# Performance work log

Measured on AMD Instinct MI355X. Metric: run time of the kernel, lower is better.

The kernel has to match this reference:

```python
import jax, jax.numpy as jnp
import numpy as np

B, M, D1, D2 = 1, 2048, 128, 16
NQ, NK, H, DH = 32, 128, 8, 16


def _build_index(M, nq, nk):
    """Replicates AttentionIndex._create_attention_idx (numpy)."""
    half = (nq - 1.0) * 0.5
    centers = np.round(np.arange(half, M + half, nq, dtype=np.float32)).astype(np.int64)
    C = len(centers)
    query_idx = np.arange(M, dtype=np.int64)
    pad = np.full(C * nq - M, -1, dtype=np.int64)
    query_idx = np.concatenate([query_idx, pad]).reshape(C, nq)
    query_mask = (query_idx != -1).astype(np.int64)
    query_idx = query_idx * query_mask
    key_idx = np.full((C, nk), -1, dtype=np.int64)
    for i, c in enumerate(centers):
        s = max(int(c) - nk // 2, 0)
        e = min(int(c) + nk // 2, M)
        key_idx[i, : e - s] = np.arange(s, e, dtype=np.int64)
    key_mask = (key_idx != -1).astype(np.int64)
    key_idx = key_idx * key_mask
    alpha_mask = query_mask[:, :, None] * key_mask[:, None, :]
    # valid slots hold flat pair index q*M + k, zero elsewhere (matches np.put_along_axis path)
    pair_idx = (query_idx[:, :, None] * M + key_idx[:, None, :]) * alpha_mask
    return query_idx, query_mask, key_idx, key_mask, alpha_mask, pair_idx


def setup_inputs() -> dict:
    key = jax.random.key(0)
    ks = jax.random.split(key, 8)
    qi, qm, ki, km, am, pi = _build_index(M, NQ, NK)
    s = 0.02
    return {
        "ql": jax.random.normal(ks[0], (B, M, D1), jnp.float32),
        "cl": jax.random.normal(ks[1], (B, M, D1), jnp.float32),
        "plm": jax.random.normal(ks[2], (B, M, M, D2), jnp.float32),
        "Wq": jax.random.normal(ks[3], (D1, H * DH), jnp.float32) * s,
        "Wk": jax.random.normal(ks[4], (D1, H * DH), jnp.float32) * s,
        "Wv": jax.random.normal(ks[5], (D1, H * DH), jnp.float32) * s,
        "Wb": jax.random.normal(ks[6], (D2, H), jnp.float32) * s,
        "Wo": jax.random.normal(ks[7], (H * DH, D1), jnp.float32) * s,
        "query_idx": jnp.asarray(qi),
        "query_mask": jnp.asarray(qm),
        "key_idx": jnp.asarray(ki),
        "key_mask": jnp.asarray(km),
        "alpha_mask": jnp.asarray(am),
        "pair_idx": jnp.asarray(pi),
    }


def _ln(x):
    mu = jnp.mean(x, axis=-1, keepdims=True)
    var = jnp.var(x, axis=-1, keepdims=True)
    return (x - mu) * jax.lax.rsqrt(var + 1e-5)


def reference(ql, cl, plm, Wq, Wk, Wv, Wb, Wo,
              query_idx, query_mask, key_idx, key_mask, alpha_mask, pair_idx):
    Bn, Mn, _ = ql.shape
    C, nq = query_idx.shape
    nk = key_idx.shape[1]
    # beta bias: 0 at valid (q,k) pairs, -1e10 at masked slots (per AtomTransformer.forward)
    beta = jnp.where(alpha_mask == 1, 0.0, -1e10).astype(ql.dtype)  # (C,nq,nk)

    q = (_ln(ql) @ Wq).reshape(Bn, Mn, H, DH)
    kv = _ln(cl)
    k = (kv @ Wk).reshape(Bn, Mn, H, DH)
    v = (kv @ Wv).reshape(Bn, Mn, H, DH)

    qw = q[:, query_idx]  # (B,C,nq,H,DH)  gather query windows
    kw = k[:, key_idx]    # (B,C,nk,H,DH)  gather key windows
    vw = v[:, key_idx]    # (B,C,nk,H,DH)

    # per-pair bias: gather plm rows via precomputed flat pair_idx
    pw = plm.reshape(Bn, Mn * Mn, D2)[:, pair_idx.reshape(-1)]
    pw = pw.reshape(Bn, C, nq, nk, D2)
    bias = jnp.moveaxis(pw @ Wb, -1, 1)  # (B,H,C,nq,nk)

    scores = jnp.einsum("bcqhd,bckhd->bhcqk", qw, kw) / np.float32(np.sqrt(DH))
    scores = scores + bias + beta[None, None]
    attn = jax.nn.softmax(scores, axis=-1)
    ow = jnp.einsum("bhcqk,bckhd->bcqhd", attn, vw)

    # scatter window outputs back to atoms (query windows tile [0,M))
    ow = ow.reshape(Bn, C * nq, H * DH) * query_mask.reshape(1, C * nq, 1).astype(ow.dtype)
    o = jnp.zeros((Bn, Mn, H * DH), ow.dtype).at[:, query_idx.reshape(-1)].add(ow)
    return ql + o @ Wo
```

## Files before the change

### kernel.cpp

```cpp
#include <hip/hip_runtime.h>
#include <math.h>

#define MDIM 2048
#define D1C  128
#define D2C  16
#define NQC  32
#define NKC  128
#define HC   8
#define DHC  16
#define CC   64

__global__ __launch_bounds__(256) void ln_proj_kernel(
    const float* __restrict__ ql, const float* __restrict__ cl,
    const float* __restrict__ Wq, const float* __restrict__ Wk,
    const float* __restrict__ Wv,
    float* __restrict__ qbuf, float* __restrict__ kbuf, float* __restrict__ vbuf)
{
    __shared__ float ldsQ[8 * 128];
    __shared__ float ldsC[8 * 128];
    const int tid = threadIdx.x;
    const int rg = tid >> 5;
    const int t  = tid & 31;
    const int m  = blockIdx.x * 8 + rg;

    const float4 xq = reinterpret_cast<const float4*>(ql)[m * 32 + t];
    const float4 xc = reinterpret_cast<const float4*>(cl)[m * 32 + t];
    float sQ  = xq.x + xq.y + xq.z + xq.w;
    float sqQ = xq.x*xq.x + xq.y*xq.y + xq.z*xq.z + xq.w*xq.w;
    float sC  = xc.x + xc.y + xc.z + xc.w;
    float sqC = xc.x*xc.x + xc.y*xc.y + xc.z*xc.z + xc.w*xc.w;
    #pragma unroll
    for (int msk = 16; msk; msk >>= 1) {
        sQ  += __shfl_xor(sQ,  msk);
        sqQ += __shfl_xor(sqQ, msk);
        sC  += __shfl_xor(sC,  msk);
        sqC += __shfl_xor(sqC, msk);
    }
    const float muQ = sQ * (1.0f / 128.0f);
    const float rsQ = rsqrtf(sqQ * (1.0f / 128.0f) - muQ * muQ + 1e-5f);
    const float muC = sC * (1.0f / 128.0f);
    const float rsC = rsqrtf(sqC * (1.0f / 128.0f) - muC * muC + 1e-5f);

    reinterpret_cast<float4*>(ldsQ)[rg * 32 + t] =
        make_float4((xq.x - muQ) * rsQ, (xq.y - muQ) * rsQ,
                    (xq.z - muQ) * rsQ, (xq.w - muQ) * rsQ);
    reinterpret_cast<float4*>(ldsC)[rg * 32 + t] =
        make_float4((xc.x - muC) * rsC, (xc.y - muC) * rsC,
                    (xc.z - muC) * rsC, (xc.w - muC) * rsC);
    __syncthreads();

    const int j   = tid & 127;
    const int rg2 = tid >> 7;
    const int r0  = rg2 * 4;
    float aq[4] = {0,0,0,0}, ak[4] = {0,0,0,0}, av[4] = {0,0,0,0};
    const float4* lq4 = reinterpret_cast<const float4*>(ldsQ);
    const float4* lc4 = reinterpret_cast<const float4*>(ldsC);
    for (int i4 = 0; i4 < 32; ++i4) {
        const int i = i4 * 4;
        const float wq0 = Wq[(i+0)*128 + j], wq1 = Wq[(i+1)*128 + j];
        const float wq2 = Wq[(i+2)*128 + j], wq3 = Wq[(i+3)*128 + j];
        const float wk0 = Wk[(i+0)*128 + j], wk1 = Wk[(i+1)*128 + j];
        const float wk2 = Wk[(i+2)*128 + j], wk3 = Wk[(i+3)*128 + j];
        const float wv0 = Wv[(i+0)*128 + j], wv1 = Wv[(i+1)*128 + j];
        const float wv2 = Wv[(i+2)*128 + j], wv3 = Wv[(i+3)*128 + j];
        #pragma unroll
        for (int rr = 0; rr < 4; ++rr) {
            const float4 x = lq4[(r0 + rr) * 32 + i4];
            aq[rr] = fmaf(x.x, wq0, fmaf(x.y, wq1, fmaf(x.z, wq2, fmaf(x.w, wq3, aq[rr]))));
            const float4 y = lc4[(r0 + rr) * 32 + i4];
            ak[rr] = fmaf(y.x, wk0, fmaf(y.y, wk1, fmaf(y.z, wk2, fmaf(y.w, wk3, ak[rr]))));
            av[rr] = fmaf(y.x, wv0, fmaf(y.y, wv1, fmaf(y.z, wv2, fmaf(y.w, wv3, av[rr]))));
        }
    }
    #pragma unroll
    for (int rr = 0; rr < 4; ++rr) {
        const int mm = blockIdx.x * 8 + r0 + rr;
        qbuf[(size_t)mm * 128 + j] = aq[rr];
        kbuf[(size_t)mm * 128 + j] = ak[rr];
        vbuf[(size_t)mm * 128 + j] = av[rr];
    }
}

__global__ __launch_bounds__(128) void bias_kernel(
    const float* __restrict__ plm, const float* __restrict__ Wb,
    const int* __restrict__ query_idx, const int* __restrict__ key_idx,
    float* __restrict__ biasBuf)
{
    __shared__ float wb[128];
    const int tid = threadIdx.x;
    wb[tid] = Wb[tid];
    const int cq = blockIdx.x;
    const int c = cq >> 5, q = cq & 31;
    const int qi = query_idx[cq];
    const int ki = key_idx[c * 128 + tid];
    __syncthreads();

    const size_t base = ((size_t)qi * 2048 + (size_t)ki) * 16;
    const float4* p4 = reinterpret_cast<const float4*>(plm + base);
    const float4 r0 = p4[0], r1 = p4[1], r2 = p4[2], r3 = p4[3];
    const float rowv[16] = { r0.x, r0.y, r0.z, r0.w, r1.x, r1.y, r1.z, r1.w,
                             r2.x, r2.y, r2.z, r2.w, r3.x, r3.y, r3.z, r3.w };
    #pragma unroll
    for (int h = 0; h < 8; ++h) {
        float acc = 0.0f;
        #pragma unroll
        for (int d = 0; d < 16; ++d) acc = fmaf(rowv[d], wb[d * 8 + h], acc);
        biasBuf[((size_t)((c * 8 + h) * 32 + q)) * 128 + tid] = acc;
    }
}

__global__ __launch_bounds__(256) void attn_kernel(
    const float* __restrict__ qbuf, const float* __restrict__ kbuf,
    const float* __restrict__ vbuf, const float* __restrict__ biasBuf,
    const int* __restrict__ query_idx, const int* __restrict__ query_mask,
    const int* __restrict__ key_idx, const int* __restrict__ key_mask,
    float* __restrict__ obuf)
{
    __shared__ float kw[128 * 20];
    __shared__ float vw[128 * 20];
    const int bid = blockIdx.x;
    const int c = bid >> 3, h = bid & 7;
    const int tid = threadIdx.x;

    for (int idx = tid; idx < 512; idx += 256) {
        const int k = idx >> 2, f = idx & 3;
        const int ki = key_idx[c * 128 + k];
        const float4 kv = reinterpret_cast<const float4*>(
            kbuf + (size_t)ki * 128 + h * 16)[f];
        *reinterpret_cast<float4*>(&kw[k * 20 + f * 4]) = kv;
        const float4 vv = reinterpret_cast<const float4*>(
            vbuf + (size_t)ki * 128 + h * 16)[f];
        *reinterpret_cast<float4*>(&vw[k * 20 + f * 4]) = vv;
    }

    const int q = tid >> 3, ks = tid & 7;
    const int qrow = query_idx[c * 32 + q];
    float qr[16];
    {
        const float4* qb4 = reinterpret_cast<const float4*>(
            qbuf + (size_t)qrow * 128 + h * 16);
        #pragma unroll
        for (int f = 0; f < 4; ++f) {
            const float4 v = qb4[f];
            qr[f*4+0] = v.x; qr[f*4+1] = v.y; qr[f*4+2] = v.z; qr[f*4+3] = v.w;
        }
    }
    __syncthreads();

    const float* bias = biasBuf + ((size_t)((c * 8 + h) * 32 + q)) * 128;
    float sarr[16];
    float mloc = -1e30f;
    #pragma unroll
    for (int j = 0; j < 16; ++j) {
        const int k = ks + 8 * j;
        const float* kr = &kw[k * 20];
        float dot = 0.0f;
        #pragma unroll
        for (int d = 0; d < 16; ++d) dot = fmaf(qr[d], kr[d], dot);
        float sc = fmaf(dot, 0.25f, bias[k]);
        sc = key_mask[c * 128 + k] ? sc : -1e30f;
        sarr[j] = sc;
        mloc = fmaxf(mloc, sc);
    }
    #pragma unroll
    for (int msk = 1; msk < 8; msk <<= 1) mloc = fmaxf(mloc, __shfl_xor(mloc, msk));

    float l = 0.0f;
    float p[16];
    #pragma unroll
    for (int j = 0; j < 16; ++j) { p[j] = __expf(sarr[j] - mloc); l += p[j]; }
    #pragma unroll
    for (int msk = 1; msk < 8; msk <<= 1) l += __shfl_xor(l, msk);

    float acc[16];
    #pragma unroll
    for (int d = 0; d < 16; ++d) acc[d] = 0.0f;
    #pragma unroll
    for (int j = 0; j < 16; ++j) {
        const int k = ks + 8 * j;
        const float* vr = &vw[k * 20];
        const float pj = p[j];
        #pragma unroll
        for (int d = 0; d < 16; ++d) acc[d] = fmaf(pj, vr[d], acc[d]);
    }
    #pragma unroll
    for (int msk = 1; msk < 8; msk <<= 1) {
        #pragma unroll
        for (int d = 0; d < 16; ++d) acc[d] += __shfl_xor(acc[d], msk);
    }
    if (ks == 0) {
        const float scale = (1.0f / l) * (float)query_mask[c * 32 + q];
        float4* ob = reinterpret_cast<float4*>(
            obuf + (size_t)(c * 32 + q) * 128 + h * 16);
        #pragma unroll
        for (int f = 0; f < 4; ++f)
            ob[f] = make_float4(acc[f*4+0]*scale, acc[f*4+1]*scale,
                                acc[f*4+2]*scale, acc[f*4+3]*scale);
    }
}

__global__ __launch_bounds__(256) void out_proj_kernel(
    const float* __restrict__ obuf, const float* __restrict__ Wo,
    const float* __restrict__ ql, float* __restrict__ out)
{
    __shared__ float ldsO[8 * 128];
    const int tid = threadIdx.x;
    reinterpret_cast<float4*>(ldsO)[tid] =
        reinterpret_cast<const float4*>(obuf)[blockIdx.x * 256 + tid];
    __syncthreads();

    const int j   = tid & 127;
    const int rg2 = tid >> 7;
    const int r0  = rg2 * 4;
    float acc[4] = {0,0,0,0};
    const float4* lo4 = reinterpret_cast<const float4*>(ldsO);
    for (int i4 = 0; i4 < 32; ++i4) {
        const int i = i4 * 4;
        const float w0 = Wo[(i+0)*128 + j], w1 = Wo[(i+1)*128 + j];
        const float w2 = Wo[(i+2)*128 + j], w3 = Wo[(i+3)*128 + j];
        #pragma unroll
        for (int rr = 0; rr < 4; ++rr) {
            const float4 x = lo4[(r0 + rr) * 32 + i4];
            acc[rr] = fmaf(x.x, w0, fmaf(x.y, w1, fmaf(x.z, w2, fmaf(x.w, w3, acc[rr]))));
        }
    }
    #pragma unroll
    for (int rr = 0; rr < 4; ++rr) {
        const int m = blockIdx.x * 8 + r0 + rr;
        out[(size_t)m * 128 + j] = ql[(size_t)m * 128 + j] + acc[rr];
    }
}

extern "C" void kernel_launch(void* const* d_in, const int* in_sizes, int n_in,
                              void* d_out, int out_size, void* d_ws, size_t ws_size,
                              hipStream_t stream) {
    const float* ql  = (const float*)d_in[0];
    const float* cl  = (const float*)d_in[1];
    const float* plm = (const float*)d_in[2];
    const float* Wq  = (const float*)d_in[3];
    const float* Wk  = (const float*)d_in[4];
    const float* Wv  = (const float*)d_in[5];
    const float* Wb  = (const float*)d_in[6];
    const float* Wo  = (const float*)d_in[7];
    const int* query_idx  = (const int*)d_in[8];
    const int* query_mask = (const int*)d_in[9];
    const int* key_idx    = (const int*)d_in[10];
    const int* key_mask   = (const int*)d_in[11];
    float* out = (float*)d_out;

    float* ws = (float*)d_ws;
    float* qbuf    = ws;
    float* kbuf    = ws + 262144;
    float* vbuf    = ws + 524288;
    float* obuf    = ws + 786432;
    float* biasBuf = ws + 1048576;

    ln_proj_kernel<<<256, 256, 0, stream>>>(ql, cl, Wq, Wk, Wv, qbuf, kbuf, vbuf);
    bias_kernel<<<2048, 128, 0, stream>>>(plm, Wb, query_idx, key_idx, biasBuf);
    attn_kernel<<<512, 256, 0, stream>>>(qbuf, kbuf, vbuf, biasBuf,
                                         query_idx, query_mask, key_idx, key_mask,
                                         obuf);
    out_proj_kernel<<<256, 256, 0, stream>>>(obuf, Wo, ql, out);
}
```

Measured before the change: 357.9 us.

## Fuse pair-bias projection into attention kernel, removing bias buffer round-trip

Result: no change. 361.8 us (+1.1%).

```diff
diff --git a/kernel.cpp b/kernel.cpp
--- a/kernel.cpp
+++ b/kernel.cpp
@@ -81,46 +81,23 @@
     }
 }
 
-__global__ __launch_bounds__(128) void bias_kernel(
-    const float* __restrict__ plm, const float* __restrict__ Wb,
-    const int* __restrict__ query_idx, const int* __restrict__ key_idx,
-    float* __restrict__ biasBuf)
-{
-    __shared__ float wb[128];
-    const int tid = threadIdx.x;
-    wb[tid] = Wb[tid];
-    const int cq = blockIdx.x;
-    const int c = cq >> 5, q = cq & 31;
-    const int qi = query_idx[cq];
-    const int ki = key_idx[c * 128 + tid];
-    __syncthreads();
-
-    const size_t base = ((size_t)qi * 2048 + (size_t)ki) * 16;
-    const float4* p4 = reinterpret_cast<const float4*>(plm + base);
-    const float4 r0 = p4[0], r1 = p4[1], r2 = p4[2], r3 = p4[3];
-    const float rowv[16] = { r0.x, r0.y, r0.z, r0.w, r1.x, r1.y, r1.z, r1.w,
-                             r2.x, r2.y, r2.z, r2.w, r3.x, r3.y, r3.z, r3.w };
-    #pragma unroll
-    for (int h = 0; h < 8; ++h) {
-        float acc = 0.0f;
-        #pragma unroll
-        for (int d = 0; d < 16; ++d) acc = fmaf(rowv[d], wb[d * 8 + h], acc);
-        biasBuf[((size_t)((c * 8 + h) * 32 + q)) * 128 + tid] = acc;
-    }
-}
-
-__global__ __launch_bounds__(256) void attn_kernel(
+__global__ __launch_bounds__(256) void attn_fused_kernel(
     const float* __restrict__ qbuf, const float* __restrict__ kbuf,
-    const float* __restrict__ vbuf, const float* __restrict__ biasBuf,
+    const float* __restrict__ vbuf, const float* __restrict__ plm,
+    const float* __restrict__ Wb,
     const int* __restrict__ query_idx, const int* __restrict__ query_mask,
     const int* __restrict__ key_idx, const int* __restrict__ key_mask,
     float* __restrict__ obuf)
 {
     __shared__ float kw[128 * 20];
     __shared__ float vw[128 * 20];
+    __shared__ float bias[32 * 132];
+    __shared__ float wb[128];
     const int bid = blockIdx.x;
-    const int c = bid >> 3, h = bid & 7;
+    const int c = bid & 63, h = bid >> 6;
     const int tid = threadIdx.x;
+
+    if (tid < 128) wb[tid] = Wb[tid];
 
     for (int idx = tid; idx < 512; idx += 256) {
         const int k = idx >> 2, f = idx & 3;
@@ -132,6 +109,28 @@
             vbuf + (size_t)ki * 128 + h * 16)[f];
         *reinterpret_cast<float4*>(&vw[k * 20 + f * 4]) = vv;
     }
+    __syncthreads();
+
+    #pragma unroll
+    for (int it = 0; it < 16; ++it) {
+        const int p = it * 256 + tid;
+        const int q = p >> 7, k = p & 127;
+        const int qi = query_idx[c * 32 + q];
+        const int ki = key_idx[c * 128 + k];
+        const size_t base = ((size_t)qi * 2048 + (size_t)ki) * 16;
+        const float4* p4 = reinterpret_cast<const float4*>(plm + base);
+        const float4 r0 = p4[0], r1 = p4[1], r2 = p4[2], r3 = p4[3];
+        float acc = 0.0f;
+        acc = fmaf(r0.x, wb[0*8+h], acc);  acc = fmaf(r0.y, wb[1*8+h], acc);
+        acc = fmaf(r0.z, wb[2*8+h], acc);  acc = fmaf(r0.w, wb[3*8+h], acc);
+        acc = fmaf(r1.x, wb[4*8+h], acc);  acc = fmaf(r1.y, wb[5*8+h], acc);
+        acc = fmaf(r1.z, wb[6*8+h], acc);  acc = fmaf(r1.w, wb[7*8+h], acc);
+        acc = fmaf(r2.x, wb[8*8+h], acc);  acc = fmaf(r2.y, wb[9*8+h], acc);
+        acc = fmaf(r2.z, wb[10*8+h], acc); acc = fmaf(r2.w, wb[11*8+h], acc);
+        acc = fmaf(r3.x, wb[12*8+h], acc); acc = fmaf(r3.y, wb[13*8+h], acc);
+        acc = fmaf(r3.z, wb[14*8+h], acc); acc = fmaf(r3.w, wb[15*8+h], acc);
+        bias[q * 132 + k] = acc;
+    }
 
     const int q = tid >> 3, ks = tid & 7;
     const int qrow = query_idx[c * 32 + q];
@@ -147,7 +146,6 @@
     }
     __syncthreads();
 
-    const float* bias = biasBuf + ((size_t)((c * 8 + h) * 32 + q)) * 128;
     float sarr[16];
     float mloc = -1e30f;
     #pragma unroll
@@ -157,7 +155,7 @@
         float dot = 0.0f;
         #pragma unroll
         for (int d = 0; d < 16; ++d) dot = fmaf(qr[d], kr[d], dot);
-        float sc = fmaf(dot, 0.25f, bias[k]);
+        float sc = fmaf(dot, 0.25f, bias[q * 132 + k]);
         sc = key_mask[c * 128 + k] ? sc : -1e30f;
         sarr[j] = sc;
         mloc = fmaxf(mloc, sc);
@@ -253,12 +251,10 @@
     float* kbuf    = ws + 262144;
     float* vbuf    = ws + 524288;
     float* obuf    = ws + 786432;
-    float* biasBuf = ws + 1048576;
 
     ln_proj_kernel<<<256, 256, 0, stream>>>(ql, cl, Wq, Wk, Wv, qbuf, kbuf, vbuf);
-    bias_kernel<<<2048, 128, 0, stream>>>(plm, Wb, query_idx, key_idx, biasBuf);
-    attn_kernel<<<512, 256, 0, stream>>>(qbuf, kbuf, vbuf, biasBuf,
-                                         query_idx, query_mask, key_idx, key_mask,
-                                         obuf);
+    attn_fused_kernel<<<512, 256, 0, stream>>>(qbuf, kbuf, vbuf, plm, Wb,
+                                               query_idx, query_mask,
+                                               key_idx, key_mask, obuf);
     out_proj_kernel<<<256, 256, 0, stream>>>(obuf, Wo, ql, out);
 }
```
